# Kernel optimization log

Hardware: AMD Instinct MI355X
Metric: run time of the kernel (lower is better)

Reference implementation:

```python
import jax, jax.numpy as jnp
import numpy as np
import math

D = 128
LAMBDA_INIT = 0.8 - 0.6 * math.exp(-0.3 * 1)  # depth=1


def _clin(xr, xi, wr, wi, br, bi):
    # complex linear: (xr + i xi) @ (wr + i wi)^T + (br + i bi)
    o_r = jnp.einsum('bhsd,od->bhso', xr, wr) - jnp.einsum('bhsd,od->bhso', xi, wi) + br
    o_i = jnp.einsum('bhsd,od->bhso', xr, wi) + jnp.einsum('bhsd,od->bhso', xi, wr) + bi
    return o_r, o_i


def setup_inputs() -> dict:
    key = jax.random.key(0)
    ks = jax.random.split(key, 32)
    B, H, S = 1, 12, 1024
    shp = (B, H, S, D)
    inp = {}
    names = ['q_r', 'q_i', 'k_r', 'k_i', 'v_r', 'v_i', 'pe_q_r', 'pe_q_i', 'pe_k_r', 'pe_k_i']
    for i, n in enumerate(names):
        inp[n] = jax.random.normal(ks[i], shp, dtype=jnp.float32)
    std = 1.0 / math.sqrt(D)
    inp['qw_r'] = jax.random.normal(ks[10], (2 * D, D), jnp.float32) * std
    inp['qw_i'] = jax.random.normal(ks[11], (2 * D, D), jnp.float32) * std
    inp['qb_r'] = jnp.zeros((2 * D,), jnp.float32)
    inp['qb_i'] = jnp.zeros((2 * D,), jnp.float32)
    for j, p in enumerate(['k', 'v', 'g', 'o']):
        inp[p + 'w_r'] = jax.random.normal(ks[12 + 2 * j], (D, D), jnp.float32) * std
        inp[p + 'w_i'] = jax.random.normal(ks[13 + 2 * j], (D, D), jnp.float32) * std
        inp[p + 'b_r'] = jnp.zeros((D,), jnp.float32)
        inp[p + 'b_i'] = jnp.zeros((D,), jnp.float32)
    inp['lq1'] = jax.random.normal(ks[20], (D,), jnp.float32) * 0.1
    inp['lk1'] = jax.random.normal(ks[21], (D,), jnp.float32) * 0.1
    inp['lq2'] = jax.random.normal(ks[22], (D,), jnp.float32) * 0.1
    inp['lk2'] = jax.random.normal(ks[23], (D,), jnp.float32) * 0.1
    inp['sub_w'] = jnp.ones((2 * D,), jnp.float32)
    return inp


def _forward(q_r, q_i, k_r, k_i, v_r, v_i, pe_q_r, pe_q_i, pe_k_r, pe_k_i,
             qw_r, qw_i, qb_r, qb_i, kw_r, kw_i, kb_r, kb_i,
             vw_r, vw_i, vb_r, vb_i, gw_r, gw_i, gb_r, gb_i,
             ow_r, ow_i, ob_r, ob_i, lq1, lk1, lq2, lk2, sub_w):
    scale = D ** (-0.5)
    qp_r, qp_i = _clin(q_r, q_i, qw_r, qw_i, qb_r, qb_i)   # [B,H,S,2D]
    kp_r, kp_i = _clin(k_r, k_i, kw_r, kw_i, kb_r, kb_i)   # [B,H,S,D]
    vp_r, vp_i = _clin(v_r, v_i, vw_r, vw_i, vb_r, vb_i)
    qp_r = qp_r + jnp.concatenate([pe_q_r, pe_q_r], axis=-1)
    qp_i = qp_i + jnp.concatenate([pe_q_i, pe_q_i], axis=-1)
    kp_r = kp_r + pe_k_r
    kp_i = kp_i + pe_k_i
    q1_r, q2_r = jnp.split(qp_r, 2, axis=-1)
    q1_i, q2_i = jnp.split(qp_i, 2, axis=-1)

    def attn_w(qr, qi):
        s_r = jnp.einsum('bhqd,bhkd->bhqk', qr, kp_r) + jnp.einsum('bhqd,bhkd->bhqk', qi, kp_i)
        s_i = jnp.einsum('bhqd,bhkd->bhqk', qi, kp_r) - jnp.einsum('bhqd,bhkd->bhqk', qr, kp_i)
        mag = jnp.sqrt(s_r ** 2 + s_i ** 2 + 1e-8) * scale
        return jax.nn.softmax(mag.astype(jnp.float32), axis=-1).astype(s_r.dtype)

    w1 = attn_w(q1_r, q1_i)
    w2 = attn_w(q2_r, q2_i)
    a1_r = jnp.einsum('bhqk,bhkd->bhqd', w1, vp_r)
    a1_i = jnp.einsum('bhqk,bhkd->bhqd', w1, vp_i)
    a2_r = jnp.einsum('bhqk,bhkd->bhqd', w2, vp_r)
    a2_i = jnp.einsum('bhqk,bhkd->bhqd', w2, vp_i)
    cat_r = jnp.concatenate([a1_r, a2_r], axis=-1)
    cat_i = jnp.concatenate([a1_i, a2_i], axis=-1)
    rms = jnp.sqrt(jnp.mean(cat_r ** 2 + cat_i ** 2, axis=-1, keepdims=True) + 1e-5)
    cat_r = cat_r / rms * sub_w
    cat_i = cat_i / rms * sub_w
    a1_r, a2_r = jnp.split(cat_r, 2, axis=-1)
    a1_i, a2_i = jnp.split(cat_i, 2, axis=-1)
    lam1 = jnp.exp(jnp.sum(lq1 * lk1))
    lam2 = jnp.exp(jnp.sum(lq2 * lk2))
    lam = jax.nn.sigmoid(lam1 - lam2 + LAMBDA_INIT)
    out_r = a1_r - lam * a2_r
    out_i = a1_i - lam * a2_i
    g_r, g_i = _clin(q_r, q_i, gw_r, gw_i, gb_r, gb_i)
    out_r, out_i = g_r * out_r - g_i * out_i, g_r * out_i + g_i * out_r
    out_r, out_i = _clin(out_r, out_i, ow_r, ow_i, ob_r, ob_i)
    return out_r, out_i


def reference(q_r, q_i, k_r, k_i, v_r, v_i, pe_q_r, pe_q_i, pe_k_r, pe_k_i,
              qw_r, qw_i, qb_r, qb_i, kw_r, kw_i, kb_r, kb_i,
              vw_r, vw_i, vb_r, vb_i, gw_r, gw_i, gb_r, gb_i,
              ow_r, ow_i, ob_r, ob_i, lq1, lk1, lq2, lk2, sub_w):
    return _forward(q_r, q_i, k_r, k_i, v_r, v_i, pe_q_r, pe_q_i, pe_k_r, pe_k_i,
                    qw_r, qw_i, qb_r, qb_i, kw_r, kw_i, kb_r, kb_i,
                    vw_r, vw_i, vb_r, vb_i, gw_r, gw_i, gb_r, gb_i,
                    ow_r, ow_i, ob_r, ob_i, lq1, lk1, lq2, lk2, sub_w)
```

## Files before the change

### kernel.cpp

```cpp
#include <hip/hip_runtime.h>
#include <math.h>

#define H 12
#define S 1024
#define D 128
#define NROWS (H * S)

typedef __attribute__((ext_vector_type(8))) _Float16 f16x8;
typedef __attribute__((ext_vector_type(4))) float f32x4;
typedef __attribute__((ext_vector_type(4))) int i32x4;

__device__ __forceinline__ short f2h(float f) {
    _Float16 h = (_Float16)f;
    return __builtin_bit_cast(short, h);
}
__device__ __forceinline__ float h2f(short s) {
    return (float)__builtin_bit_cast(_Float16, s);
}
__device__ __forceinline__ f16x8 fneg8(f16x8 v) {
    i32x4 u = __builtin_bit_cast(i32x4, v);
    u ^= (int)0x80008000;
    return __builtin_bit_cast(f16x8, u);
}

#define WS_QP_R   0ULL
#define WS_QP_I   6291456ULL
#define WS_KP_R   12582912ULL
#define WS_KP_I   15728640ULL
#define WS_VPT_R  18874368ULL
#define WS_VPT_I  22020096ULL
#define WS_GP_R   25165824ULL
#define WS_GP_I   28311552ULL
#define WS_ACAT_R 31457280ULL
#define WS_ACAT_I 37748736ULL
#define WS_LAM    44040192ULL
#define WS_SC     44040448ULL
#define W16_PER_HEAD   4194304ULL
#define STAT_PER_HEAD  16384ULL

__global__ void lam_kernel(const float* __restrict__ lq1, const float* __restrict__ lk1,
                           const float* __restrict__ lq2, const float* __restrict__ lk2,
                           float* __restrict__ lam_out)
{
    int t = threadIdx.x;
    float p1 = lq1[t] * lk1[t];
    float p2 = lq2[t] * lk2[t];
    #pragma unroll
    for (int off = 32; off; off >>= 1) {
        p1 += __shfl_xor(p1, off);
        p2 += __shfl_xor(p2, off);
    }
    __shared__ float s1[2], s2[2];
    if ((t & 63) == 0) { s1[t >> 6] = p1; s2[t >> 6] = p2; }
    __syncthreads();
    if (t == 0) {
        float l1 = expf(s1[0] + s1[1]);
        float l2 = expf(s2[0] + s2[1]);
        float x = l1 - l2 + 0.3555090675909693f;
        lam_out[0] = 1.0f / (1.0f + expf(-x));
    }
}

__global__ __launch_bounds__(256) void proj_all(
    const float* __restrict__ q_r, const float* __restrict__ q_i,
    const float* __restrict__ k_r, const float* __restrict__ k_i,
    const float* __restrict__ v_r, const float* __restrict__ v_i,
    const float* __restrict__ pe_q_r, const float* __restrict__ pe_q_i,
    const float* __restrict__ pe_k_r, const float* __restrict__ pe_k_i,
    const float* __restrict__ qw_r, const float* __restrict__ qw_i,
    const float* __restrict__ qb_r, const float* __restrict__ qb_i,
    const float* __restrict__ kw_r, const float* __restrict__ kw_i,
    const float* __restrict__ kb_r, const float* __restrict__ kb_i,
    const float* __restrict__ vw_r, const float* __restrict__ vw_i,
    const float* __restrict__ vb_r, const float* __restrict__ vb_i,
    const float* __restrict__ gw_r, const float* __restrict__ gw_i,
    const float* __restrict__ gb_r, const float* __restrict__ gb_i,
    short* __restrict__ qp_r, short* __restrict__ qp_i,
    short* __restrict__ kp_r, short* __restrict__ kp_i,
    short* __restrict__ vpT_r, short* __restrict__ vpT_i,
    short* __restrict__ gp_r, short* __restrict__ gp_i)
{
    const int y = blockIdx.y;
    const float *xr, *xi, *wr, *wi, *br, *bi, *per = nullptr, *pei = nullptr;
    short *outr_, *outi_;
    int M, omode, col0;
    if (y < 4)      { xr = q_r; xi = q_i; wr = qw_r; wi = qw_i; br = qb_r; bi = qb_i;
                      per = pe_q_r; pei = pe_q_i; outr_ = qp_r; outi_ = qp_i;
                      M = 256; omode = 1; col0 = y * 64; }
    else if (y < 6) { xr = k_r; xi = k_i; wr = kw_r; wi = kw_i; br = kb_r; bi = kb_i;
                      per = pe_k_r; pei = pe_k_i; outr_ = kp_r; outi_ = kp_i;
                      M = 128; omode = 1; col0 = (y - 4) * 64; }
    else if (y < 8) { xr = v_r; xi = v_i; wr = vw_r; wi = vw_i; br = vb_r; bi = vb_i;
                      outr_ = vpT_r; outi_ = vpT_i;
                      M = 128; omode = 2; col0 = (y - 6) * 64; }
    else            { xr = q_r; xi = q_i; wr = gw_r; wi = gw_i; br = gb_r; bi = gb_i;
                      outr_ = gp_r; outi_ = gp_i;
                      M = 128; omode = 1; col0 = (y - 8) * 64; }

    __shared__ short As[64 * 72], Brs[64 * 72], Bis[64 * 72];
    const int t = threadIdx.x;
    const int row0 = blockIdx.x * 64;
    const int lane = t & 63, wid = t >> 6;
    const int wm = (wid >> 1) * 32, wn = (wid & 1) * 32;
    const int fm = lane & 15, fq = lane >> 4;
    f32x4 zero4 = {0.f, 0.f, 0.f, 0.f};
    f32x4 accr[2][2], acci[2][2];
    #pragma unroll
    for (int i = 0; i < 2; ++i)
        #pragma unroll
        for (int j = 0; j < 2; ++j) { accr[i][j] = zero4; acci[i][j] = zero4; }

    for (int c = 0; c < 4; ++c) {
        const bool hi = (c >= 2);
        const int kb = (c & 1) * 64;
        const float* Asrc = hi ? xi : xr;
        const float* Brsrc = hi ? wi : wr;
        const float* Bisrc = hi ? wr : wi;
        const float bsign = hi ? -1.0f : 1.0f;
        __syncthreads();
        #pragma unroll
        for (int it = 0; it < 4; ++it) {
            int lin = it * 256 + t;
            int r = lin >> 4, k4 = (lin & 15) * 4;
            float4 va = *(const float4*)&Asrc[(size_t)(row0 + r) * 128 + kb + k4];
            *(short4*)&As[r * 72 + k4] = make_short4(f2h(va.x), f2h(va.y), f2h(va.z), f2h(va.w));
            float4 vr = *(const float4*)&Brsrc[(size_t)(col0 + r) * 128 + kb + k4];
            *(short4*)&Brs[r * 72 + k4] = make_short4(f2h(bsign * vr.x), f2h(bsign * vr.y),
                                                      f2h(bsign * vr.z), f2h(bsign * vr.w));
            float4 vi = *(const float4*)&Bisrc[(size_t)(col0 + r) * 128 + kb + k4];
            *(short4*)&Bis[r * 72 + k4] = make_short4(f2h(vi.x), f2h(vi.y), f2h(vi.z), f2h(vi.w));
        }
        __syncthreads();
        #pragma unroll
        for (int ks = 0; ks < 64; ks += 32) {
            f16x8 bfr[2], bfi[2];
            #pragma unroll
            for (int j = 0; j < 2; ++j) {
                bfr[j] = *(const f16x8*)&Brs[(wn + j * 16 + fm) * 72 + ks + fq * 8];
                bfi[j] = *(const f16x8*)&Bis[(wn + j * 16 + fm) * 72 + ks + fq * 8];
            }
            #pragma unroll
            for (int i = 0; i < 2; ++i) {
                f16x8 a = *(const f16x8*)&As[(wm + i * 16 + fm) * 72 + ks + fq * 8];
                #pragma unroll
                for (int j = 0; j < 2; ++j) {
                    accr[i][j] = __builtin_amdgcn_mfma_f32_16x16x32_f16(a, bfr[j], accr[i][j], 0, 0, 0);
                    acci[i][j] = __builtin_amdgcn_mfma_f32_16x16x32_f16(a, bfi[j], acci[i][j], 0, 0, 0);
                }
            }
        }
    }
    #pragma unroll
    for (int i = 0; i < 2; ++i)
        #pragma unroll
        for (int j = 0; j < 2; ++j) {
            int colc = col0 + wn + j * 16 + fm;
            float bbr = br[colc], bbi = bi[colc];
            if (omode == 2) {
                int rb = row0 + wm + i * 16 + fq * 4;
                int hq = rb >> 10, sq = rb & 1023;
                short4 o_r4 = make_short4(f2h(accr[i][j][0] + bbr), f2h(accr[i][j][1] + bbr),
                                          f2h(accr[i][j][2] + bbr), f2h(accr[i][j][3] + bbr));
                short4 o_i4 = make_short4(f2h(acci[i][j][0] + bbi), f2h(acci[i][j][1] + bbi),
                                          f2h(acci[i][j][2] + bbi), f2h(acci[i][j][3] + bbi));
                size_t ob = ((size_t)(hq * 128 + colc)) * 1024 + sq;
                *(short4*)&outr_[ob] = o_r4;
                *(short4*)&outi_[ob] = o_i4;
            } else {
                #pragma unroll
                for (int reg = 0; reg < 4; ++reg) {
                    int rr = row0 + wm + i * 16 + fq * 4 + reg;
                    float o_r = accr[i][j][reg] + bbr;
                    float o_i = acci[i][j][reg] + bbi;
                    if (per) {
                        o_r += per[(size_t)rr * 128 + (colc & 127)];
                        o_i += pei[(size_t)rr * 128 + (colc & 127)];
                    }
                    outr_[(size_t)rr * M + colc] = f2h(o_r);
                    outi_[(size_t)rr * M + colc] = f2h(o_i);
                }
            }
        }
}

__global__ __launch_bounds__(256) void oproj_mfma(
    const short* __restrict__ gp_r, const short* __restrict__ gp_i,
    const float* __restrict__ wr, const float* __restrict__ wi,
    const float* __restrict__ br, const float* __restrict__ bi,
    float* __restrict__ outr, float* __restrict__ outi)
{
    __shared__ short As[64 * 72], Brs[64 * 72], Bis[64 * 72];
    const int t = threadIdx.x;
    const int row0 = blockIdx.x * 64, col0 = blockIdx.y * 64;
    const int lane = t & 63, wid = t >> 6;
    const int wm = (wid >> 1) * 32, wn = (wid & 1) * 32;
    const int fm = lane & 15, fq = lane >> 4;
    f32x4 zero4 = {0.f, 0.f, 0.f, 0.f};
    f32x4 accr[2][2], acci[2][2];
    #pragma unroll
    for (int i = 0; i < 2; ++i)
        #pragma unroll
        for (int j = 0; j < 2; ++j) { accr[i][j] = zero4; acci[i][j] = zero4; }

    for (int c = 0; c < 4; ++c) {
        const bool hi = (c >= 2);
        const int kb = (c & 1) * 64;
        const short* Asrc = hi ? gp_i : gp_r;
        const float* Brsrc = hi ? wi : wr;
        const float* Bisrc = hi ? wr : wi;
        const float bsign = hi ? -1.0f : 1.0f;
        __syncthreads();
        #pragma unroll
        for (int it = 0; it < 4; ++it) {
            int lin = it * 256 + t;
            int r = lin >> 4, k4 = (lin & 15) * 4;
            *(short4*)&As[r * 72 + k4] = *(const short4*)&Asrc[(size_t)(row0 + r) * 128 + kb + k4];
            float4 vr = *(const float4*)&Brsrc[(size_t)(col0 + r) * 128 + kb + k4];
            *(short4*)&Brs[r * 72 + k4] = make_short4(f2h(bsign * vr.x), f2h(bsign * vr.y),
                                                      f2h(bsign * vr.z), f2h(bsign * vr.w));
            float4 vi = *(const float4*)&Bisrc[(size_t)(col0 + r) * 128 + kb + k4];
            *(short4*)&Bis[r * 72 + k4] = make_short4(f2h(vi.x), f2h(vi.y), f2h(vi.z), f2h(vi.w));
        }
        __syncthreads();
        #pragma unroll
        for (int ks = 0; ks < 64; ks += 32) {
            f16x8 bfr[2], bfi[2];
            #pragma unroll
            for (int j = 0; j < 2; ++j) {
                bfr[j] = *(const f16x8*)&Brs[(wn + j * 16 + fm) * 72 + ks + fq * 8];
                bfi[j] = *(const f16x8*)&Bis[(wn + j * 16 + fm) * 72 + ks + fq * 8];
            }
            #pragma unroll
            for (int i = 0; i < 2; ++i) {
                f16x8 a = *(const f16x8*)&As[(wm + i * 16 + fm) * 72 + ks + fq * 8];
                #pragma unroll
                for (int j = 0; j < 2; ++j) {
                    accr[i][j] = __builtin_amdgcn_mfma_f32_16x16x32_f16(a, bfr[j], accr[i][j], 0, 0, 0);
                    acci[i][j] = __builtin_amdgcn_mfma_f32_16x16x32_f16(a, bfi[j], acci[i][j], 0, 0, 0);
                }
            }
        }
    }
    #pragma unroll
    for (int i = 0; i < 2; ++i)
        #pragma unroll
        for (int j = 0; j < 2; ++j) {
            int colc = col0 + wn + j * 16 + fm;
            float bbr = br[colc], bbi = bi[colc];
            #pragma unroll
            for (int reg = 0; reg < 4; ++reg) {
                int rr = row0 + wm + i * 16 + fq * 4 + reg;
                outr[(size_t)rr * 128 + colc] = accr[i][j][reg] + bbr;
                outi[(size_t)rr * 128 + colc] = acci[i][j][reg] + bbi;
            }
        }
}

__global__ __launch_bounds__(256) void score_mfma(
    const short* __restrict__ qp_r, const short* __restrict__ qp_i,
    const short* __restrict__ kp_r, const short* __restrict__ kp_i,
    short* __restrict__ w16, int h0)
{
    __shared__ short Qr[64 * 72], Qi[64 * 72], Kt[128 * 72];
    const int t = threadIdx.x;
    const int hh = blockIdx.z >> 1, map = blockIdx.z & 1;
    const int h = h0 + hh;
    const int q0 = blockIdx.x * 64, c0 = blockIdx.y * 128;
    const int lane = t & 63, wid = t >> 6;
    const int wm = (wid >> 1) * 32, wn = (wid & 1) * 64;
    const int fm = lane & 15, fq = lane >> 4;
    f32x4 zero4 = {0.f, 0.f, 0.f, 0.f};
    f32x4 sr[2][4], si[2][4];
    #pragma unroll
    for (int i = 0; i < 2; ++i)
        #pragma unroll
        for (int j = 0; j < 4; ++j) { sr[i][j] = zero4; si[i][j] = zero4; }

    for (int kb = 0; kb < 2; ++kb) {
        const int kbase = map * 128 + kb * 64;
        __syncthreads();
        #pragma unroll
        for (int i = 0; i < 4; ++i) {
            int lin = i * 256 + t;
            int r = lin >> 4, k4 = (lin & 15) * 4;
            size_t qb = (size_t)(h * S + q0 + r) * 256 + kbase + k4;
            *(short4*)&Qr[r * 72 + k4] = *(const short4*)&qp_r[qb];
            *(short4*)&Qi[r * 72 + k4] = *(const short4*)&qp_i[qb];
        }
        #pragma unroll
        for (int i = 0; i < 8; ++i) {
            int lin = i * 256 + t;
            int r = lin >> 4, k4 = (lin & 15) * 4;
            *(short4*)&Kt[r * 72 + k4] =
                *(const short4*)&kp_r[(size_t)(h * S + c0 + r) * 128 + kb * 64 + k4];
        }
        __syncthreads();
        f16x8 aR[2][2], aI[2][2];
        #pragma unroll
        for (int ks = 0; ks < 2; ++ks)
            #pragma unroll
            for (int i = 0; i < 2; ++i) {
                int ao = (wm + i * 16 + fm) * 72 + ks * 32 + fq * 8;
                aR[ks][i] = *(const f16x8*)&Qr[ao];
                aI[ks][i] = *(const f16x8*)&Qi[ao];
            }
        #pragma unroll
        for (int ks = 0; ks < 2; ++ks) {
            f16x8 b[4];
            #pragma unroll
            for (int j = 0; j < 4; ++j)
                b[j] = *(const f16x8*)&Kt[(wn + j * 16 + fm) * 72 + ks * 32 + fq * 8];
            #pragma unroll
            for (int i = 0; i < 2; ++i)
                #pragma unroll
                for (int j = 0; j < 4; ++j) {
                    sr[i][j] = __builtin_amdgcn_mfma_f32_16x16x32_f16(aR[ks][i], b[j], sr[i][j], 0, 0, 0);
                    si[i][j] = __builtin_amdgcn_mfma_f32_16x16x32_f16(aI[ks][i], b[j], si[i][j], 0, 0, 0);
                }
        }
        __syncthreads();
        #pragma unroll
        for (int i = 0; i < 8; ++i) {
            int lin = i * 256 + t;
            int r = lin >> 4, k4 = (lin & 15) * 4;
            *(short4*)&Kt[r * 72 + k4] =
                *(const short4*)&kp_i[(size_t)(h * S + c0 + r) * 128 + kb * 64 + k4];
        }
        __syncthreads();
        #pragma unroll
        for (int ks = 0; ks < 2; ++ks) {
            f16x8 b[4];
            #pragma unroll
            for (int j = 0; j < 4; ++j)
                b[j] = *(const f16x8*)&Kt[(wn + j * 16 + fm) * 72 + ks * 32 + fq * 8];
            f16x8 nR0 = fneg8(aR[ks][0]), nR1 = fneg8(aR[ks][1]);
            #pragma unroll
            for (int j = 0; j < 4; ++j) {
                sr[0][j] = __builtin_amdgcn_mfma_f32_16x16x32_f16(aI[ks][0], b[j], sr[0][j], 0, 0, 0);
                si[0][j] = __builtin_amdgcn_mfma_f32_16x16x32_f16(nR0, b[j], si[0][j], 0, 0, 0);
                sr[1][j] = __builtin_amdgcn_mfma_f32_16x16x32_f16(aI[ks][1], b[j], sr[1][j], 0, 0, 0);
                si[1][j] = __builtin_amdgcn_mfma_f32_16x16x32_f16(nR1, b[j], si[1][j], 0, 0, 0);
            }
        }
    }
    const float scale = 0.08838834764831845f;
    #pragma unroll
    for (int i = 0; i < 2; ++i)
        #pragma unroll
        for (int j = 0; j < 4; ++j) {
            int kcol = c0 + wn + j * 16 + fm;
            #pragma unroll
            for (int reg = 0; reg < 4; ++reg) {
                int q = q0 + wm + i * 16 + fq * 4 + reg;
                float r1 = sr[i][j][reg], I1 = si[i][j][reg];
                float m1 = sqrtf(fmaf(r1, r1, fmaf(I1, I1, 1e-8f))) * scale;
                w16[(((size_t)hh * 2 + map) * S + q) * S + kcol] = f2h(m1);
            }
        }
}

__global__ __launch_bounds__(256) void smstats(const short* __restrict__ w16,
                                               float2* __restrict__ stats)
{
    const short* row = w16 + (size_t)blockIdx.x * S;
    int t = threadIdx.x;
    short4 s = ((const short4*)row)[t];
    float f0 = h2f(s.x), f1 = h2f(s.y), f2v = h2f(s.z), f3 = h2f(s.w);
    float m = fmaxf(fmaxf(f0, f1), fmaxf(f2v, f3));
    #pragma unroll
    for (int off = 32; off; off >>= 1) m = fmaxf(m, __shfl_xor(m, off));
    __shared__ float redm[4], reds[4];
    int w = t >> 6;
    if ((t & 63) == 0) redm[w] = m;
    __syncthreads();
    m = fmaxf(fmaxf(redm[0], redm[1]), fmaxf(redm[2], redm[3]));
    float ssum = __expf(f0 - m) + __expf(f1 - m) + __expf(f2v - m) + __expf(f3 - m);
    #pragma unroll
    for (int off = 32; off; off >>= 1) ssum += __shfl_xor(ssum, off);
    if ((t & 63) == 0) reds[w] = ssum;
    __syncthreads();
    if (t == 0) {
        float total = reds[0] + reds[1] + reds[2] + reds[3];
        stats[blockIdx.x] = make_float2(m, 1.0f / total);
    }
}

__global__ __launch_bounds__(256) void av_mfma(
    const short* __restrict__ w16, const float2* __restrict__ stats,
    const short* __restrict__ vpT_r, const short* __restrict__ vpT_i,
    short* __restrict__ acat_r, short* __restrict__ acat_i, int h0)
{
    __shared__ short W1[32 * 72], W2[32 * 72], Vc[128 * 72];
    const int t = threadIdx.x;
    const int hh = blockIdx.z, h = h0 + hh;
    const int comp = blockIdx.y;
    const int q0 = blockIdx.x * 32;
    const short* vpT = comp ? vpT_i : vpT_r;
    short* acat = comp ? acat_i : acat_r;
    const float2* st1 = stats + ((size_t)hh * 2 + 0) * S;
    const float2* st2 = stats + ((size_t)hh * 2 + 1) * S;
    const int lane = t & 63, wid = t >> 6;
    const int wm = (wid >> 1) * 16, wn = (wid & 1) * 64;
    const int fm = lane & 15, fq = lane >> 4;
    f32x4 zero4 = {0.f, 0.f, 0.f, 0.f};
    f32x4 a1[4], a2[4];
    #pragma unroll
    for (int j = 0; j < 4; ++j) { a1[j] = zero4; a2[j] = zero4; }

    for (int k0 = 0; k0 < S; k0 += 64) {
        __syncthreads();
        #pragma unroll
        for (int it = 0; it < 2; ++it) {
            int lin = it * 256 + t;
            int r = lin >> 4, k4 = (lin & 15) * 4;
            float2 s1v = st1[q0 + r];
            float2 s2v = st2[q0 + r];
            short4 m1 = *(const short4*)&w16[(((size_t)hh * 2 + 0) * S + q0 + r) * S + k0 + k4];
            short4 m2 = *(const short4*)&w16[(((size_t)hh * 2 + 1) * S + q0 + r) * S + k0 + k4];
            *(short4*)&W1[r * 72 + k4] = make_short4(
                f2h(__expf(h2f(m1.x) - s1v.x) * s1v.y), f2h(__expf(h2f(m1.y) - s1v.x) * s1v.y),
                f2h(__expf(h2f(m1.z) - s1v.x) * s1v.y), f2h(__expf(h2f(m1.w) - s1v.x) * s1v.y));
            *(short4*)&W2[r * 72 + k4] = make_short4(
                f2h(__expf(h2f(m2.x) - s2v.x) * s2v.y), f2h(__expf(h2f(m2.y) - s2v.x) * s2v.y),
                f2h(__expf(h2f(m2.z) - s2v.x) * s2v.y), f2h(__expf(h2f(m2.w) - s2v.x) * s2v.y));
        }
        #pragma unroll
        for (int it = 0; it < 8; ++it) {
            int lin = it * 256 + t;
            int dd = lin >> 4, k4 = (lin & 15) * 4;
            *(short4*)&Vc[dd * 72 + k4] = *(const short4*)&vpT[(size_t)(h * 128 + dd) * 1024 + k0 + k4];
        }
        __syncthreads();
        #pragma unroll
        for (int ks = 0; ks < 64; ks += 32) {
            f16x8 b[4];
            #pragma unroll
            for (int j = 0; j < 4; ++j)
                b[j] = *(const f16x8*)&Vc[(wn + j * 16 + fm) * 72 + ks + fq * 8];
            int wo = (wm + fm) * 72 + ks + fq * 8;
            f16x8 w1f = *(const f16x8*)&W1[wo];
            f16x8 w2f = *(const f16x8*)&W2[wo];
            #pragma unroll
            for (int j = 0; j < 4; ++j) {
                a1[j] = __builtin_amdgcn_mfma_f32_16x16x32_f16(w1f, b[j], a1[j], 0, 0, 0);
                a2[j] = __builtin_amdgcn_mfma_f32_16x16x32_f16(w2f, b[j], a2[j], 0, 0, 0);
            }
        }
    }
    #pragma unroll
    for (int j = 0; j < 4; ++j) {
        int d = wn + j * 16 + fm;
        #pragma unroll
        for (int reg = 0; reg < 4; ++reg) {
            int q = q0 + wm + fq * 4 + reg;
            size_t rowb = (size_t)(h * S + q) * 256;
            acat[rowb + d]       = f2h(a1[j][reg]);
            acat[rowb + 128 + d] = f2h(a2[j][reg]);
        }
    }
}

__global__ __launch_bounds__(256) void rmsgate_kernel(
    const short* __restrict__ acat_r, const short* __restrict__ acat_i,
    const float* __restrict__ sub_w, const float* __restrict__ lam_ptr,
    short* __restrict__ gp_r, short* __restrict__ gp_i)
{
    int row = blockIdx.x;
    int t = threadIdx.x;
    float ar = h2f(acat_r[(size_t)row * 256 + t]);
    float ai = h2f(acat_i[(size_t)row * 256 + t]);
    float ss = fmaf(ar, ar, ai * ai);
    #pragma unroll
    for (int off = 32; off; off >>= 1) ss += __shfl_xor(ss, off);
    __shared__ float red[4];
    if ((t & 63) == 0) red[t >> 6] = ss;
    __syncthreads();
    float total = red[0] + red[1] + red[2] + red[3];
    float inv_rms = 1.0f / sqrtf(total * (1.0f / 256.0f) + 1e-5f);
    float sw = sub_w[t];
    __shared__ float Cr[256], Ci[256];
    Cr[t] = ar * inv_rms * sw;
    Ci[t] = ai * inv_rms * sw;
    __syncthreads();
    if (t < 128) {
        float lam = lam_ptr[0];
        float o_r = Cr[t] - lam * Cr[t + 128];
        float o_i = Ci[t] - lam * Ci[t + 128];
        float gr = h2f(gp_r[(size_t)row * 128 + t]);
        float gi = h2f(gp_i[(size_t)row * 128 + t]);
        gp_r[(size_t)row * 128 + t] = f2h(gr * o_r - gi * o_i);
        gp_i[(size_t)row * 128 + t] = f2h(gr * o_i + gi * o_r);
    }
}

extern "C" void kernel_launch(void* const* d_in, const int* in_sizes, int n_in,
                              void* d_out, int out_size, void* d_ws, size_t ws_size,
                              hipStream_t stream)
{
    (void)in_sizes; (void)n_in; (void)out_size;
    const float* q_r    = (const float*)d_in[0];
    const float* q_i    = (const float*)d_in[1];
    const float* k_r    = (const float*)d_in[2];
    const float* k_i    = (const float*)d_in[3];
    const float* v_r    = (const float*)d_in[4];
    const float* v_i    = (const float*)d_in[5];
    const float* pe_q_r = (const float*)d_in[6];
    const float* pe_q_i = (const float*)d_in[7];
    const float* pe_k_r = (const float*)d_in[8];
    const float* pe_k_i = (const float*)d_in[9];
    const float* qw_r   = (const float*)d_in[10];
    const float* qw_i   = (const float*)d_in[11];
    const float* qb_r   = (const float*)d_in[12];
    const float* qb_i   = (const float*)d_in[13];
    const float* kw_r   = (const float*)d_in[14];
    const float* kw_i   = (const float*)d_in[15];
    const float* kb_r   = (const float*)d_in[16];
    const float* kb_i   = (const float*)d_in[17];
    const float* vw_r   = (const float*)d_in[18];
    const float* vw_i   = (const float*)d_in[19];
    const float* vb_r   = (const float*)d_in[20];
    const float* vb_i   = (const float*)d_in[21];
    const float* gw_r   = (const float*)d_in[22];
    const float* gw_i   = (const float*)d_in[23];
    const float* gb_r   = (const float*)d_in[24];
    const float* gb_i   = (const float*)d_in[25];
    const float* ow_r   = (const float*)d_in[26];
    const float* ow_i   = (const float*)d_in[27];
    const float* ob_r   = (const float*)d_in[28];
    const float* ob_i   = (const float*)d_in[29];
    const float* lq1    = (const float*)d_in[30];
    const float* lk1    = (const float*)d_in[31];
    const float* lq2    = (const float*)d_in[32];
    const float* lk2    = (const float*)d_in[33];
    const float* sub_w  = (const float*)d_in[34];

    char* ws = (char*)d_ws;
    short* qp_r   = (short*)(ws + WS_QP_R);
    short* qp_i   = (short*)(ws + WS_QP_I);
    short* kp_r   = (short*)(ws + WS_KP_R);
    short* kp_i   = (short*)(ws + WS_KP_I);
    short* vpT_r  = (short*)(ws + WS_VPT_R);
    short* vpT_i  = (short*)(ws + WS_VPT_I);
    short* gp_r   = (short*)(ws + WS_GP_R);
    short* gp_i   = (short*)(ws + WS_GP_I);
    short* acat_r = (short*)(ws + WS_ACAT_R);
    short* acat_i = (short*)(ws + WS_ACAT_I);
    float* lam    = (float*)(ws + WS_LAM);
    short* w16    = (short*)(ws + WS_SC);

    float* out_r = (float*)d_out;
    float* out_i = out_r + (size_t)NROWS * D;

    size_t avail = ws_size > WS_SC ? ws_size - WS_SC : 0;
    int nh_chunk = (int)(avail / (W16_PER_HEAD + STAT_PER_HEAD));
    if (nh_chunk < 1) nh_chunk = 1;
    if (nh_chunk > H) nh_chunk = H;
    float2* stats = (float2*)(ws + WS_SC + (size_t)nh_chunk * W16_PER_HEAD);

    lam_kernel<<<1, 128, 0, stream>>>(lq1, lk1, lq2, lk2, lam);

    proj_all<<<dim3(192, 10), 256, 0, stream>>>(
        q_r, q_i, k_r, k_i, v_r, v_i, pe_q_r, pe_q_i, pe_k_r, pe_k_i,
        qw_r, qw_i, qb_r, qb_i, kw_r, kw_i, kb_r, kb_i,
        vw_r, vw_i, vb_r, vb_i, gw_r, gw_i, gb_r, gb_i,
        qp_r, qp_i, kp_r, kp_i, vpT_r, vpT_i, gp_r, gp_i);

    for (int h0 = 0; h0 < H; h0 += nh_chunk) {
        int nhh = (H - h0 < nh_chunk) ? (H - h0) : nh_chunk;
        score_mfma<<<dim3(16, 8, nhh * 2), 256, 0, stream>>>(qp_r, qp_i, kp_r, kp_i, w16, h0);
        smstats<<<nhh * 2 * S, 256, 0, stream>>>(w16, stats);
        av_mfma<<<dim3(32, 2, nhh), 256, 0, stream>>>(w16, stats, vpT_r, vpT_i, acat_r, acat_i, h0);
    }

    rmsgate_kernel<<<NROWS, 256, 0, stream>>>(acat_r, acat_i, sub_w, lam, gp_r, gp_i);

    oproj_mfma<<<dim3(192, 2), 256, 0, stream>>>(gp_r, gp_i, ow_r, ow_i, ob_r, ob_i, out_r, out_i);
}
```

Before: 296.7 us.

## Fuse softmax row statistics into score kernel with partial max/sum combine

The score kernel now computes per-tile row max and exp-sum partials from its fp32 magnitudes and writes them to a small partial buffer. A lightweight combine kernel merges the 16 partials per row into the final max and inverse sum. This replaces the separate smstats pass, which re-read the whole fp16 score matrix. It also computes the statistics from fp32 values instead of fp16-rounded ones, so they may differ slightly from the stored weights.

```diff
diff --git a/kernel.cpp b/kernel.cpp
--- a/kernel.cpp
+++ b/kernel.cpp
@@ -37,6 +37,7 @@
 #define WS_SC     44040448ULL
 #define W16_PER_HEAD   4194304ULL
 #define STAT_PER_HEAD  16384ULL
+#define PART_PER_HEAD  262144ULL
 
 __global__ void lam_kernel(const float* __restrict__ lq1, const float* __restrict__ lk1,
                            const float* __restrict__ lq2, const float* __restrict__ lk2,
@@ -259,7 +260,7 @@
 __global__ __launch_bounds__(256) void score_mfma(
     const short* __restrict__ qp_r, const short* __restrict__ qp_i,
     const short* __restrict__ kp_r, const short* __restrict__ kp_i,
-    short* __restrict__ w16, int h0)
+    short* __restrict__ w16, float2* __restrict__ partial, int h0)
 {
     __shared__ short Qr[64 * 72], Qi[64 * 72], Kt[128 * 72];
     const int t = threadIdx.x;
@@ -354,35 +355,43 @@
                 int q = q0 + wm + i * 16 + fq * 4 + reg;
                 float r1 = sr[i][j][reg], I1 = si[i][j][reg];
                 float m1 = sqrtf(fmaf(r1, r1, fmaf(I1, I1, 1e-8f))) * scale;
+                sr[i][j][reg] = m1;
                 w16[(((size_t)hh * 2 + map) * S + q) * S + kcol] = f2h(m1);
             }
         }
-}
-
-__global__ __launch_bounds__(256) void smstats(const short* __restrict__ w16,
-                                               float2* __restrict__ stats)
-{
-    const short* row = w16 + (size_t)blockIdx.x * S;
-    int t = threadIdx.x;
-    short4 s = ((const short4*)row)[t];
-    float f0 = h2f(s.x), f1 = h2f(s.y), f2v = h2f(s.z), f3 = h2f(s.w);
-    float m = fmaxf(fmaxf(f0, f1), fmaxf(f2v, f3));
-    #pragma unroll
-    for (int off = 32; off; off >>= 1) m = fmaxf(m, __shfl_xor(m, off));
-    __shared__ float redm[4], reds[4];
-    int w = t >> 6;
-    if ((t & 63) == 0) redm[w] = m;
-    __syncthreads();
-    m = fmaxf(fmaxf(redm[0], redm[1]), fmaxf(redm[2], redm[3]));
-    float ssum = __expf(f0 - m) + __expf(f1 - m) + __expf(f2v - m) + __expf(f3 - m);
-    #pragma unroll
-    for (int off = 32; off; off >>= 1) ssum += __shfl_xor(ssum, off);
-    if ((t & 63) == 0) reds[w] = ssum;
-    __syncthreads();
-    if (t == 0) {
-        float total = reds[0] + reds[1] + reds[2] + reds[3];
-        stats[blockIdx.x] = make_float2(m, 1.0f / total);
-    }
+    #pragma unroll
+    for (int i = 0; i < 2; ++i)
+        #pragma unroll
+        for (int reg = 0; reg < 4; ++reg) {
+            float mx = fmaxf(fmaxf(sr[i][0][reg], sr[i][1][reg]),
+                             fmaxf(sr[i][2][reg], sr[i][3][reg]));
+            #pragma unroll
+            for (int off = 1; off < 16; off <<= 1) mx = fmaxf(mx, __shfl_xor(mx, off));
+            float sm = __expf(sr[i][0][reg] - mx) + __expf(sr[i][1][reg] - mx)
+                     + __expf(sr[i][2][reg] - mx) + __expf(sr[i][3][reg] - mx);
+            #pragma unroll
+            for (int off = 1; off < 16; off <<= 1) sm += __shfl_xor(sm, off);
+            if (fm == 0) {
+                int q = q0 + wm + i * 16 + fq * 4 + reg;
+                size_t prow = ((size_t)hh * 2 + map) * S + q;
+                partial[prow * 16 + blockIdx.y * 2 + (wn >> 6)] = make_float2(mx, sm);
+            }
+        }
+}
+
+__global__ __launch_bounds__(256) void smcombine(const float2* __restrict__ partial,
+                                                 float2* __restrict__ stats)
+{
+    int row = blockIdx.x * 256 + threadIdx.x;
+    const float2* p = partial + (size_t)row * 16;
+    float2 p0 = p[0];
+    float m = p0.x;
+    #pragma unroll
+    for (int b = 1; b < 16; ++b) m = fmaxf(m, p[b].x);
+    float l = 0.f;
+    #pragma unroll
+    for (int b = 0; b < 16; ++b) l += p[b].y * __expf(p[b].x - m);
+    stats[row] = make_float2(m, 1.0f / l);
 }
 
 __global__ __launch_bounds__(256) void av_mfma(
@@ -552,10 +561,11 @@
     float* out_i = out_r + (size_t)NROWS * D;
 
     size_t avail = ws_size > WS_SC ? ws_size - WS_SC : 0;
-    int nh_chunk = (int)(avail / (W16_PER_HEAD + STAT_PER_HEAD));
+    int nh_chunk = (int)(avail / (W16_PER_HEAD + STAT_PER_HEAD + PART_PER_HEAD));
     if (nh_chunk < 1) nh_chunk = 1;
     if (nh_chunk > H) nh_chunk = H;
-    float2* stats = (float2*)(ws + WS_SC + (size_t)nh_chunk * W16_PER_HEAD);
+    float2* stats   = (float2*)(ws + WS_SC + (size_t)nh_chunk * W16_PER_HEAD);
+    float2* partial = (float2*)(ws + WS_SC + (size_t)nh_chunk * (W16_PER_HEAD + STAT_PER_HEAD));
 
     lam_kernel<<<1, 128, 0, stream>>>(lq1, lk1, lq2, lk2, lam);
 
@@ -567,8 +577,8 @@
 
     for (int h0 = 0; h0 < H; h0 += nh_chunk) {
         int nhh = (H - h0 < nh_chunk) ? (H - h0) : nh_chunk;
-        score_mfma<<<dim3(16, 8, nhh * 2), 256, 0, stream>>>(qp_r, qp_i, kp_r, kp_i, w16, h0);
-        smstats<<<nhh * 2 * S, 256, 0, stream>>>(w16, stats);
+        score_mfma<<<dim3(16, 8, nhh * 2), 256, 0, stream>>>(qp_r, qp_i, kp_r, kp_i, w16, partial, h0);
+        smcombine<<<nhh * 8, 256, 0, stream>>>(partial, stats);
         av_mfma<<<dim3(32, 2, nhh), 256, 0, stream>>>(w16, stats, vpT_r, vpT_i, acat_r, acat_i, h0);
     }
 
```

After: 303.9 us. 2.4% more time.
